# Performance work log

Measured on AMD Instinct MI355X. Metric: run time of the kernel, lower is better.

## Reference

```python
import jax, jax.numpy as jnp
import numpy as np

INV_TEMP = 20.0
THRESHOLD = 0.01
SING_CUTOFF = 3.0
D0 = 128  # order-0 descriptor block
EPS = 1e-6


def setup_inputs() -> dict:
    key = jax.random.key(0)
    ks = jax.random.split(key, 6)
    B, N, M, D = 4, 4096, 4096, 256
    K = (D - D0) // 2
    return {
        "keypoints_A": jax.random.uniform(ks[0], (B, N, 2), jnp.float32) * 2.0 - 1.0,
        "descriptions_A": jax.random.normal(ks[1], (B, N, D), jnp.float32),
        "keypoints_B": jax.random.uniform(ks[2], (B, M, 2), jnp.float32) * 2.0 - 1.0,
        "descriptions_B": jax.random.normal(ks[3], (B, M, D), jnp.float32),
        "W_lstsq": jax.random.normal(ks[4], (D0, K), jnp.float32) * 0.1,
        "b_lstsq": jnp.zeros((K,), jnp.float32),
    }


def _svdvals_2x2(A):
    # singular values of [..,2,2] via eigenvalues of A^T A (closed form)
    M = jnp.einsum('...ki,...kj->...ij', A, A)
    t = M[..., 0, 0] + M[..., 1, 1]
    d = M[..., 0, 0] * M[..., 1, 1] - M[..., 0, 1] * M[..., 1, 0]
    disc = jnp.sqrt(jnp.maximum(0.25 * t * t - d, 0.0))
    lam_hi = 0.5 * t + disc
    lam_lo = jnp.maximum(0.5 * t - disc, 0.0)
    return jnp.sqrt(lam_hi), jnp.sqrt(lam_lo)


def reference(keypoints_A, descriptions_A, keypoints_B, descriptions_B, W_lstsq, b_lstsq):
    B, N, D = descriptions_A.shape
    K = (D - D0) // 2
    # --- dual softmax matcher (normalize=True) ---
    dA = descriptions_A / jnp.linalg.norm(descriptions_A, axis=-1, keepdims=True)
    dB = descriptions_B / jnp.linalg.norm(descriptions_B, axis=-1, keepdims=True)
    sim = INV_TEMP * jnp.einsum('bnd,bmd->bnm', dA, dB)  # [B,N,M]
    P = jax.nn.softmax(sim, axis=-2) * jax.nn.softmax(sim, axis=-1)
    # --- mutual nearest neighbors, fixed-shape (one candidate per A-row) ---
    j = jnp.argmax(P, axis=-1)  # [B,N]
    Pij = jnp.take_along_axis(P, j[..., None], axis=-1)[..., 0]
    colmax_j = jnp.take_along_axis(P.max(axis=-2), j, axis=-1)
    valid = (Pij >= colmax_j) & (Pij > THRESHOLD)  # mutual max + threshold
    # --- gather raw descriptors for matched pairs ---
    descB_m = jnp.take_along_axis(descriptions_B, j[..., None], axis=1)  # [B,N,D]
    desc0_A, desc1_A = descriptions_A[..., :D0], descriptions_A[..., D0:]
    desc0_B, desc1_B = descB_m[..., :D0], descB_m[..., D0:]
    # --- lstsq weights from order-0 features ---
    wA = jax.nn.softplus(desc0_A @ W_lstsq + b_lstsq)
    wB = jax.nn.softplus(desc0_B @ W_lstsq + b_lstsq)
    w = jnp.sqrt(wA * wB)  # [B,N,K]
    # --- weighted 2x2 affine lstsq: A x ~ y ---
    X = desc1_A.reshape(B, N, K, 2)
    Y = desc1_B.reshape(B, N, K, 2)
    G = jnp.einsum('bnk,bnki,bnkj->bnij', w, X, X) + EPS * jnp.eye(2, dtype=X.dtype)
    C = jnp.einsum('bnk,bnki,bnkj->bnij', w, Y, X)
    est = jnp.swapaxes(jnp.linalg.solve(G, jnp.swapaxes(C, -1, -2)), -1, -2)  # [B,N,2,2]
    # --- singular value / determinant filter ---
    s_hi, s_lo = _svdvals_2x2(est)
    good = jnp.isfinite(s_hi + s_lo) & (s_hi < SING_CUTOFF) & (s_lo > 1.0 / SING_CUTOFF)
    det = est[..., 0, 0] * est[..., 1, 1] - est[..., 0, 1] * est[..., 1, 0]
    good = good & (det > 0)  # remove_negative_determinants=True
    valid = valid & good
    matches_A = keypoints_A  # row i of A pairs with column j[b,i]
    matches_B = jnp.take_along_axis(keypoints_B, j[..., None], axis=1)
    return matches_A, matches_B, j, valid
```

## Files before the change

### kernel.cpp

```cpp
#include <hip/hip_runtime.h>
#include <math.h>

#define Bb   4
#define Nn   4096
#define Mm   4096
#define Dd   256
#define D0c  128
#define Kc   64

typedef _Float16 half8 __attribute__((ext_vector_type(8)));
typedef float    f32x4 __attribute__((ext_vector_type(4)));

__device__ __forceinline__ unsigned encf(float f) {
    unsigned u = __float_as_uint(f);
    return (u & 0x80000000u) ? ~u : (u | 0x80000000u);
}
__device__ __forceinline__ float decf(unsigned u) {
    return (u & 0x80000000u) ? __uint_as_float(u ^ 0x80000000u) : __uint_as_float(~u);
}
__device__ __forceinline__ float softplusf(float x) {
    return fmaxf(x, 0.f) + log1pf(expf(-fabsf(x)));
}
__device__ __forceinline__ void gl_lds16(const _Float16* g, _Float16* l) {
    __builtin_amdgcn_global_load_lds((const __attribute__((address_space(1))) void*)g,
                                     (__attribute__((address_space(3))) void*)l, 16, 0, 0);
}

__device__ __forceinline__ void decode_tile(int bid, int swz, int& mt, int& nt, int& zz) {
    if (swz == 2) {
        const int xcd = bid & 7, k = bid >> 3;
        zz = xcd >> 2;
        const int s = xcd & 3;
        mt = (s & 1) * 16 + (k & 15);
        nt = (s >> 1) * 16 + (k >> 4);
    } else if (swz == 1) {
        const int xcd = bid & 7, k = bid >> 3;
        zz = 0;
        const int s = xcd >> 1;
        const int t = (xcd & 1) * 128 + k;
        mt = (s & 1) * 16 + (t & 15);
        nt = (s >> 1) * 16 + (t >> 4);
    } else {
        mt = bid & 31; nt = (bid >> 5) & 31; zz = bid >> 10;
    }
}

__global__ __launch_bounds__(256) void prep_kernel(
    const float* __restrict__ dA, const float* __restrict__ dB,
    _Float16* __restrict__ Ah, _Float16* __restrict__ Al,
    _Float16* __restrict__ Bh, _Float16* __restrict__ Bl,
    unsigned* __restrict__ colMaxU)
{
    const int t = threadIdx.x, wave = t >> 6, lane = t & 63;
    const int row = blockIdx.x * 4 + wave;
    if (blockIdx.y == 0 && lane == 0) colMaxU[row] = 0u;
    const float* src = blockIdx.y ? dB : dA;
    _Float16* dh = blockIdx.y ? Bh : Ah;
    _Float16* dl = blockIdx.y ? Bl : Al;
    const float4 v = *(const float4*)&src[(size_t)row * Dd + lane * 4];
    float ss = v.x * v.x + v.y * v.y + v.z * v.z + v.w * v.w;
#pragma unroll
    for (int m = 32; m; m >>= 1) ss += __shfl_xor(ss, m, 64);
    const float inv = 1.0f / sqrtf(ss);
    float x[4] = {v.x * inv, v.y * inv, v.z * inv, v.w * inv};
    union { _Float16 h[4]; uint2 u; } ph, pl;
#pragma unroll
    for (int i = 0; i < 4; i++) {
        _Float16 h = (_Float16)x[i];
        ph.h[i] = h;
        pl.h[i] = (_Float16)((x[i] - (float)h) * 4096.f);
    }
    const size_t toff = (size_t)(row >> 7) * 32768
                      + (size_t)(lane >> 3) * 4096
                      + (size_t)((lane >> 1) & 3) * 1024
                      + (size_t)(row & 127) * 8 + (lane & 1) * 4;
    *(uint2*)&dh[toff] = ph.u;
    *(uint2*)&dl[toff] = pl.u;
}

template<int PB, int STORE>
__global__ __launch_bounds__(256, 2) void sim_kernel(
    const _Float16* __restrict__ Ah, const _Float16* __restrict__ Al,
    const _Float16* __restrict__ Bh, const _Float16* __restrict__ Bl,
    const float* __restrict__ Lrow_g, const float* __restrict__ Lcol_g,
    float* __restrict__ rowsumP, float* __restrict__ colsumP,
    float* __restrict__ rkey, int* __restrict__ rmArr, float* __restrict__ rcvArr,
    unsigned* __restrict__ cmU, float* __restrict__ simG, int b0, int swz)
{
    __shared__ _Float16 lds[2][4][4][128][8];
    __shared__ float    colp[128];
    __shared__ float    rowp[128];
    __shared__ unsigned colu[128];
    __shared__ float    shL[128], shLc[128];
    __shared__ float    s_bk[128], s_bc[128];
    __shared__ int      s_bm[128];

    const int t = threadIdx.x;
    const int wave = t >> 6, lane = t & 63;
    const int wr = wave >> 1, wc = wave & 1;
    int mt, nt, bbl;
    decode_tile(blockIdx.x, swz, mt, nt, bbl);
    const int bb = b0 + bbl;
    const int n0 = nt * 128, m0 = mt * 128;

    if (PB) {
        if (t < 128) {
            shL[t]  = Lrow_g[bb * Nn + n0 + t];
            shLc[t] = Lcol_g[bb * Mm + m0 + t];
            colu[t] = 0u;
        }
    } else {
        if (t < 128) { colp[t] = 0.f; rowp[t] = 0.f; }
    }

    const _Float16* gb;
    {
        const size_t offA = (size_t)(bb * Nn + n0) * Dd;
        const size_t offB = (size_t)(bb * Mm + m0) * Dd;
        if      (wave == 0) gb = Ah + offA;
        else if (wave == 1) gb = Al + offA;
        else if (wave == 2) gb = Bh + offB;
        else                gb = Bl + offB;
    }

    f32x4 acc1[4][4], acc2[4][4];
#pragma unroll
    for (int ti = 0; ti < 4; ti++)
#pragma unroll
        for (int tj = 0; tj < 4; tj++) { acc1[ti][tj] = (f32x4)0.f; acc2[ti][tj] = (f32x4)0.f; }

    const int quad = lane >> 4, l15 = lane & 15;
    _Float16* lw0 = &lds[0][wave][0][0][0];
    _Float16* lw1 = &lds[1][wave][0][0][0];

#pragma unroll
    for (int q = 0; q < 8; ++q)
        gl_lds16(gb + q * 512 + lane * 8, lw0 + q * 512);

#pragma unroll
    for (int kc8 = 0; kc8 < 8; ++kc8) {
        const int cur = kc8 & 1;
        if (kc8 < 7) {
            _Float16* nw = cur ? lw0 : lw1;
            const _Float16* gsrc = gb + (kc8 + 1) * 4096;
#pragma unroll
            for (int q = 0; q < 8; ++q)
                gl_lds16(gsrc + q * 512 + lane * 8, nw + q * 512);
            asm volatile("s_waitcnt vmcnt(8)" ::: "memory");
        } else {
            asm volatile("s_waitcnt vmcnt(0)" ::: "memory");
        }
        __builtin_amdgcn_s_barrier();
        __builtin_amdgcn_sched_barrier(0);

        half8 afh[4], afl[4];
#pragma unroll
        for (int ti = 0; ti < 4; ++ti) {
            afh[ti] = *(const half8*)&lds[cur][0][quad][wr * 64 + ti * 16 + l15][0];
            afl[ti] = *(const half8*)&lds[cur][1][quad][wr * 64 + ti * 16 + l15][0];
        }
#pragma unroll
        for (int tj = 0; tj < 4; ++tj) {
            half8 bh = *(const half8*)&lds[cur][2][quad][wc * 64 + tj * 16 + l15][0];
            half8 bl = *(const half8*)&lds[cur][3][quad][wc * 64 + tj * 16 + l15][0];
#pragma unroll
            for (int ti = 0; ti < 4; ++ti) {
                acc1[ti][tj] = __builtin_amdgcn_mfma_f32_16x16x32_f16(afh[ti], bh, acc1[ti][tj], 0, 0, 0);
                acc2[ti][tj] = __builtin_amdgcn_mfma_f32_16x16x32_f16(afh[ti], bl, acc2[ti][tj], 0, 0, 0);
                acc2[ti][tj] = __builtin_amdgcn_mfma_f32_16x16x32_f16(afl[ti], bh, acc2[ti][tj], 0, 0, 0);
            }
        }
        asm volatile("s_waitcnt lgkmcnt(0)" ::: "memory");
        __builtin_amdgcn_s_barrier();
    }

    if (!PB) {
        float rp[16] = {0.f}, cp[4] = {0.f};
#pragma unroll
        for (int ti = 0; ti < 4; ++ti)
#pragma unroll
            for (int tj = 0; tj < 4; ++tj)
#pragma unroll
                for (int r = 0; r < 4; ++r) {
                    float dot = fmaf(acc2[ti][tj][r], 2.44140625e-4f, acc1[ti][tj][r]);
                    acc1[ti][tj][r] = dot;
                    float e = __expf(fmaf(20.f, dot, -20.f));
                    rp[ti * 4 + r] += e;
                    cp[tj] += e;
                }
#pragma unroll
        for (int i = 0; i < 16; ++i)
#pragma unroll
            for (int m = 1; m < 16; m <<= 1) rp[i] += __shfl_xor(rp[i], m, 64);
        if (l15 == 0) {
#pragma unroll
            for (int ti = 0; ti < 4; ++ti)
#pragma unroll
                for (int r = 0; r < 4; ++r)
                    atomicAdd(&rowp[wr * 64 + ti * 16 + quad * 4 + r], rp[ti * 4 + r]);
        }
#pragma unroll
        for (int tj = 0; tj < 4; ++tj) {
            cp[tj] += __shfl_xor(cp[tj], 16, 64);
            cp[tj] += __shfl_xor(cp[tj], 32, 64);
        }
        if (quad == 0) {
#pragma unroll
            for (int tj = 0; tj < 4; ++tj) atomicAdd(&colp[wc * 64 + tj * 16 + l15], cp[tj]);
        }
        __syncthreads();
        if (t < 128) {
            rowsumP[(size_t)(bb * 32 + mt) * Nn + n0 + t] = rowp[t];
            colsumP[(size_t)(bb * 32 + nt) * Mm + m0 + t] = colp[t];
        }
        if (STORE) {
            float* base = simG + ((size_t)bbl * Nn + n0) * Mm + m0 + wc * 64;
#pragma unroll
            for (int ti = 0; ti < 4; ++ti)
#pragma unroll
                for (int r = 0; r < 4; ++r) {
                    float* rowp_ = base + (size_t)(wr * 64 + ti * 16 + quad * 4 + r) * Mm;
#pragma unroll
                    for (int tj = 0; tj < 4; ++tj)
                        __builtin_nontemporal_store(acc1[ti][tj][r], rowp_ + tj * 16 + l15);
                }
        }
    } else {
        float Lr[16];
#pragma unroll
        for (int ti = 0; ti < 4; ++ti)
#pragma unroll
            for (int r = 0; r < 4; ++r)
                Lr[ti * 4 + r] = shL[wr * 64 + ti * 16 + quad * 4 + r];

        float bk[16], bc[16];
        int bm[16];
        unsigned cu[4];
#pragma unroll
        for (int i = 0; i < 16; i++) { bk[i] = -INFINITY; bc[i] = -INFINITY; bm[i] = 0x7fffffff; }
#pragma unroll
        for (int j = 0; j < 4; j++) cu[j] = 0u;

#pragma unroll
        for (int ti = 0; ti < 4; ++ti)
#pragma unroll
            for (int tj = 0; tj < 4; ++tj)
#pragma unroll
                for (int r = 0; r < 4; ++r) {
                    float dot = fmaf(acc2[ti][tj][r], 2.44140625e-4f, acc1[ti][tj][r]);
                    float cv = fmaf(40.f, dot, -40.f - Lr[ti * 4 + r]);
                    float kv = cv - shLc[wc * 64 + tj * 16 + l15];
                    const int i = ti * 4 + r;
                    if (kv > bk[i]) { bk[i] = kv; bm[i] = m0 + wc * 64 + tj * 16 + l15; bc[i] = cv; }
                    unsigned e = encf(cv);
                    if (e > cu[tj]) cu[tj] = e;
                }
#pragma unroll
        for (int i = 0; i < 16; ++i) {
#pragma unroll
            for (int m = 1; m < 16; m <<= 1) {
                float okv = __shfl_xor(bk[i], m, 64);
                int   om  = __shfl_xor(bm[i], m, 64);
                float ocv = __shfl_xor(bc[i], m, 64);
                if (okv > bk[i] || (okv == bk[i] && om < bm[i])) { bk[i] = okv; bm[i] = om; bc[i] = ocv; }
            }
        }
        if (l15 == 0 && wc == 0) {
#pragma unroll
            for (int ti = 0; ti < 4; ++ti)
#pragma unroll
                for (int r = 0; r < 4; ++r) {
                    const int row = wr * 64 + ti * 16 + quad * 4 + r, i = ti * 4 + r;
                    s_bk[row] = bk[i]; s_bm[row] = bm[i]; s_bc[row] = bc[i];
                }
        }
        __syncthreads();
        if (l15 == 0 && wc == 1) {
#pragma unroll
            for (int ti = 0; ti < 4; ++ti)
#pragma unroll
                for (int r = 0; r < 4; ++r) {
                    const int row = wr * 64 + ti * 16 + quad * 4 + r, i = ti * 4 + r;
                    float k0 = s_bk[row];
                    if (bk[i] > k0 || (bk[i] == k0 && bm[i] < s_bm[row])) {
                        s_bk[row] = bk[i]; s_bm[row] = bm[i]; s_bc[row] = bc[i];
                    }
                }
        }
#pragma unroll
        for (int tj = 0; tj < 4; ++tj) {
            unsigned o = __shfl_xor(cu[tj], 16, 64); if (o > cu[tj]) cu[tj] = o;
            o = __shfl_xor(cu[tj], 32, 64); if (o > cu[tj]) cu[tj] = o;
        }
        if (quad == 0) {
#pragma unroll
            for (int tj = 0; tj < 4; ++tj) atomicMax(&colu[wc * 64 + tj * 16 + l15], cu[tj]);
        }
        __syncthreads();
        if (t < 128) {
            size_t idx = (size_t)(bb * 32 + mt) * Nn + n0 + t;
            rkey[idx] = s_bk[t]; rmArr[idx] = s_bm[t]; rcvArr[idx] = s_bc[t];
            cmU[(size_t)(bb * 32 + nt) * Mm + m0 + t] = colu[t];
        }
    }
}

__global__ __launch_bounds__(256) void logsum_kernel(
    const float* __restrict__ rowsumP, const float* __restrict__ colsumP,
    float* __restrict__ Lrow, float* __restrict__ Lcol, int b0, int CB)
{
    int t = blockIdx.x * 256 + threadIdx.x;
    int half = CB * 4096;
    int which = t >= half;
    int idx = which ? (t - half) : t;
    int bb = b0 + (idx >> 12), n = idx & 4095;
    const float* P = which ? colsumP : rowsumP;
    float s = 0.f;
    for (int mt = 0; mt < 32; ++mt) s += P[(size_t)(bb * 32 + mt) * 4096 + n];
    (which ? Lcol : Lrow)[bb * 4096 + n] = logf(s);
}

__global__ __launch_bounds__(256) void scan_kernel(
    const float* __restrict__ simG,
    const float* __restrict__ Lrow, const float* __restrict__ Lcol,
    float* __restrict__ kvP, float* __restrict__ cvP, int* __restrict__ jP,
    unsigned* __restrict__ colMaxU, int b0)
{
    __shared__ unsigned colu[1024];
    const int t = threadIdx.x, wave = t >> 6, lane = t & 63;
    const int blk = blockIdx.x;
    const int bbl = blk >> 10;
    const int r10 = blk & 1023;
    const int stripe = r10 >> 2, q = r10 & 3;
    const int bb = b0 + bbl;
    const int col0 = q * 1024;
    const int row0 = stripe * 16 + wave * 4;

    for (int i = t; i < 1024; i += 256) colu[i] = 0u;
    __syncthreads();

    f32x4 Lc4[4], cmax[4];
    const float* LcB = Lcol + bb * Mm + col0;
#pragma unroll
    for (int c = 0; c < 4; ++c) {
        Lc4[c] = *(const f32x4*)&LcB[c * 256 + lane * 4];
        cmax[c] = (f32x4)(-INFINITY);
    }

    const float* rowbase = simG + (size_t)(bbl * Nn + row0) * Mm + col0;
    f32x4 cur[4], nxt[4];
#pragma unroll
    for (int c = 0; c < 4; ++c)
        cur[c] = __builtin_nontemporal_load((const f32x4*)&rowbase[c * 256 + lane * 4]);

    for (int r = 0; r < 4; ++r) {
        if (r < 3) {
            const float* nrow = rowbase + (size_t)(r + 1) * Mm;
#pragma unroll
            for (int c = 0; c < 4; ++c)
                nxt[c] = __builtin_nontemporal_load((const f32x4*)&nrow[c * 256 + lane * 4]);
        }
        const int n = bb * Nn + row0 + r;
        const float Ln = Lrow[n];
        const float cbias = -40.f - Ln;
        float bk = -INFINITY, bc = -INFINITY;
        int bm = 0x7fffffff;
#pragma unroll
        for (int c = 0; c < 4; ++c) {
            float cv0 = fmaf(40.f, cur[c].x, cbias);
            float cv1 = fmaf(40.f, cur[c].y, cbias);
            float cv2 = fmaf(40.f, cur[c].z, cbias);
            float cv3 = fmaf(40.f, cur[c].w, cbias);
            cmax[c].x = fmaxf(cmax[c].x, cv0);
            cmax[c].y = fmaxf(cmax[c].y, cv1);
            cmax[c].z = fmaxf(cmax[c].z, cv2);
            cmax[c].w = fmaxf(cmax[c].w, cv3);
            const int mb = col0 + c * 256 + lane * 4;
            float kv0 = cv0 - Lc4[c].x;
            float kv1 = cv1 - Lc4[c].y;
            float kv2 = cv2 - Lc4[c].z;
            float kv3 = cv3 - Lc4[c].w;
            if (kv0 > bk) { bk = kv0; bm = mb;     bc = cv0; }
            if (kv1 > bk) { bk = kv1; bm = mb + 1; bc = cv1; }
            if (kv2 > bk) { bk = kv2; bm = mb + 2; bc = cv2; }
            if (kv3 > bk) { bk = kv3; bm = mb + 3; bc = cv3; }
        }
#pragma unroll
        for (int sh = 1; sh < 64; sh <<= 1) {
            float okv = __shfl_xor(bk, sh, 64);
            int   om  = __shfl_xor(bm, sh, 64);
            float ocv = __shfl_xor(bc, sh, 64);
            if (okv > bk || (okv == bk && om < bm)) { bk = okv; bm = om; bc = ocv; }
        }
        if (lane == 0) {
            size_t o = ((size_t)bb * Nn + row0 + r) * 4 + q;
            kvP[o] = bk; cvP[o] = bc; jP[o] = bm;
        }
#pragma unroll
        for (int c = 0; c < 4; ++c) cur[c] = nxt[c];
    }
#pragma unroll
    for (int c = 0; c < 4; ++c) {
        const int mb = c * 256 + lane * 4;
        atomicMax(&colu[mb],     encf(cmax[c].x));
        atomicMax(&colu[mb + 1], encf(cmax[c].y));
        atomicMax(&colu[mb + 2], encf(cmax[c].z));
        atomicMax(&colu[mb + 3], encf(cmax[c].w));
    }
    __syncthreads();
    unsigned* cm = colMaxU + (size_t)bb * Mm + col0;
    for (int i = t; i < 1024; i += 256) atomicMax(&cm[i], colu[i]);
}

__global__ __launch_bounds__(256) void validate_kernel(
    const float* __restrict__ kvP, const float* __restrict__ cvP,
    const int* __restrict__ jP, const unsigned* __restrict__ colMaxU,
    float* __restrict__ outJ, int* __restrict__ jIdx, int* __restrict__ v1)
{
    const float LOG_THR = -4.605170185988091f;
    const int p = blockIdx.x * 256 + threadIdx.x;
    const int bb = p >> 12;
    float bk = -INFINITY, bc = -INFINITY;
    int bm = 0x7fffffff;
#pragma unroll
    for (int q = 0; q < 4; ++q) {
        size_t o = (size_t)p * 4 + q;
        float k = kvP[o];
        int   m = jP[o];
        if (k > bk || (k == bk && m < bm)) { bk = k; bm = m; bc = cvP[o]; }
    }
    const float cm = decf(colMaxU[(size_t)bb * Mm + bm]);
    const int ok = (bk > LOG_THR) && (bc >= cm);
    outJ[p] = (float)bm;
    jIdx[p] = bm;
    v1[p] = ok;
}

__global__ __launch_bounds__(256) void finalize_kernel(
    const float* __restrict__ rkey, const int* __restrict__ rmArr,
    const float* __restrict__ rcvArr, const unsigned* __restrict__ cmU,
    float* __restrict__ outJ, int* __restrict__ jIdx, int* __restrict__ v1)
{
    const float LOG_THR = -4.605170185988091f;
    int p = blockIdx.x * 256 + threadIdx.x;
    int bb = p >> 12, n = p & 4095;
    float bk = -INFINITY, bc = -INFINITY;
    int bm = 0;
    for (int mt = 0; mt < 32; ++mt) {
        size_t idx = (size_t)(bb * 32 + mt) * Nn + n;
        float k = rkey[idx];
        if (k > bk) { bk = k; bm = rmArr[idx]; bc = rcvArr[idx]; }
    }
    unsigned u = 0u;
    for (int nt = 0; nt < 32; ++nt) {
        unsigned c = cmU[(size_t)(bb * 32 + nt) * Mm + bm];
        if (c > u) u = c;
    }
    float cm = decf(u);
    int ok = (bk > LOG_THR) && (bc >= cm);
    outJ[p] = (float)bm;
    jIdx[p] = bm;
    v1[p]   = ok;
}

__global__ __launch_bounds__(256) void affine_kernel(
    const float* __restrict__ descA, const float* __restrict__ descB,
    const float* __restrict__ kpA, const float* __restrict__ kpB,
    const float* __restrict__ W, const float* __restrict__ bvec,
    const int* __restrict__ jIdx, const int* __restrict__ v1,
    float* __restrict__ outA, float* __restrict__ outB, float* __restrict__ outV)
{
    __shared__ float Ws[D0c * Kc];
    __shared__ float sbuf[4][4][D0c];
    const int t = threadIdx.x, wave = t >> 6, lane = t & 63;
    for (int i = t; i < D0c * Kc; i += 256) Ws[i] = W[i];
    const float bl = bvec[lane];
    __syncthreads();

    float* s0A = sbuf[wave][0];
    float* s1A = sbuf[wave][1];
    float* s0B = sbuf[wave][2];
    float* s1B = sbuf[wave][3];

    for (int p = 0; p < 8; ++p) {
        const int point = blockIdx.x * 32 + wave * 8 + p;
        const int bb = point >> 12;
        const int j = jIdx[point];
        const float* da = descA + (size_t)point * Dd;
        const float* db = descB + (size_t)(bb * Mm + j) * Dd;
        s0A[lane] = da[lane];       s0A[64 + lane] = da[64 + lane];
        s1A[lane] = da[128 + lane]; s1A[64 + lane] = da[192 + lane];
        s0B[lane] = db[lane];       s0B[64 + lane] = db[64 + lane];
        s1B[lane] = db[128 + lane]; s1B[64 + lane] = db[192 + lane];
        __syncthreads();

        float xa = bl, xb = bl;
#pragma unroll 8
        for (int d = 0; d < 128; ++d) {
            float w_ = Ws[d * 64 + lane];
            xa = fmaf(s0A[d], w_, xa);
            xb = fmaf(s0B[d], w_, xb);
        }
        float wa = softplusf(xa), wb = softplusf(xb);
        float w = sqrtf(wa * wb);
        float x0 = s1A[2 * lane], x1 = s1A[2 * lane + 1];
        float y0 = s1B[2 * lane], y1 = s1B[2 * lane + 1];
        float g00 = w * x0 * x0, g01 = w * x0 * x1, g11 = w * x1 * x1;
        float c00 = w * y0 * x0, c01 = w * y0 * x1;
        float c10 = w * y1 * x0, c11 = w * y1 * x1;
#pragma unroll
        for (int m = 32; m; m >>= 1) {
            g00 += __shfl_xor(g00, m, 64); g01 += __shfl_xor(g01, m, 64); g11 += __shfl_xor(g11, m, 64);
            c00 += __shfl_xor(c00, m, 64); c01 += __shfl_xor(c01, m, 64);
            c10 += __shfl_xor(c10, m, 64); c11 += __shfl_xor(c11, m, 64);
        }
        if (lane == 0) {
            g00 += 1e-6f; g11 += 1e-6f;
            float det = g00 * g11 - g01 * g01;
            float e00 = (c00 * g11 - c01 * g01) / det;
            float e01 = (c01 * g00 - c00 * g01) / det;
            float e10 = (c10 * g11 - c11 * g01) / det;
            float e11 = (c11 * g00 - c10 * g01) / det;
            float m00 = e00 * e00 + e10 * e10;
            float m01 = e00 * e01 + e10 * e11;
            float m11 = e01 * e01 + e11 * e11;
            float tr = m00 + m11;
            float dm = m00 * m11 - m01 * m01;
            float disc = sqrtf(fmaxf(0.25f * tr * tr - dm, 0.f));
            float lhi = 0.5f * tr + disc;
            float llo = fmaxf(0.5f * tr - disc, 0.f);
            float shi = sqrtf(lhi), slo = sqrtf(llo);
            float sdet = e00 * e11 - e01 * e10;
            int good = isfinite(shi + slo) && (shi < 3.0f) && (slo > 0.33333334f) && (sdet > 0.f);
            int valid = v1[point] && good;
            outA[2 * point]     = kpA[2 * point];
            outA[2 * point + 1] = kpA[2 * point + 1];
            const float* kb = kpB + (size_t)(bb * Mm + j) * 2;
            outB[2 * point]     = kb[0];
            outB[2 * point + 1] = kb[1];
            outV[point] = valid ? 1.f : 0.f;
        }
        __syncthreads();
    }
}

extern "C" void kernel_launch(void* const* d_in, const int* in_sizes, int n_in,
                              void* d_out, int out_size, void* d_ws, size_t ws_size,
                              hipStream_t stream) {
    const float* kpA = (const float*)d_in[0];
    const float* dA  = (const float*)d_in[1];
    const float* kpB = (const float*)d_in[2];
    const float* dB  = (const float*)d_in[3];
    const float* W   = (const float*)d_in[4];
    const float* bl  = (const float*)d_in[5];
    float* out = (float*)d_out;

    char* ws = (char*)d_ws;
    _Float16* Ah = (_Float16*)ws;  ws += 8388608;
    _Float16* Al = (_Float16*)ws;  ws += 8388608;
    _Float16* Bh = (_Float16*)ws;  ws += 8388608;
    _Float16* Bl = (_Float16*)ws;  ws += 8388608;
    float*    rowsumP = (float*)ws;    ws += 2097152;
    float*    colsumP = (float*)ws;    ws += 2097152;
    float*    Lrow    = (float*)ws;    ws += 65536;
    float*    Lcol    = (float*)ws;    ws += 65536;
    int*      jIdx    = (int*)ws;      ws += 65536;
    int*      v1      = (int*)ws;      ws += 65536;
    float*    kvP     = (float*)ws;    ws += 262144;
    float*    cvP     = (float*)ws;    ws += 262144;
    int*      jP      = (int*)ws;      ws += 262144;
    unsigned* colMaxU = (unsigned*)ws; ws += 65536;
    char*     big     = ws;

    const size_t base = (size_t)(big - (char*)d_ws);

    float*    rkey  = (float*)big;
    int*      rmArr = (int*)(big + 2097152);
    float*    rcvArr= (float*)(big + 4194304);
    unsigned* cmU   = (unsigned*)(big + 6291456);

    float* outA = out;
    float* outB = out + 32768;
    float* outJ = out + 65536;
    float* outV = out + 81920;

    const size_t per = 67108864ull;
    int CB = 0;
    if      (ws_size >= base + 2 * per) CB = 2;
    else if (ws_size >= base + 1 * per) CB = 1;

    prep_kernel<<<dim3(4096, 2), 256, 0, stream>>>(dA, dB, Ah, Al, Bh, Bl, colMaxU);

    if (CB) {
        float* simG = (float*)big;
        for (int b0 = 0; b0 < Bb; b0 += CB) {
            sim_kernel<0, 1><<<1024 * CB, 256, 0, stream>>>(
                Ah, Al, Bh, Bl, nullptr, nullptr, rowsumP, colsumP,
                nullptr, nullptr, nullptr, nullptr, simG, b0, CB);
            logsum_kernel<<<32 * CB, 256, 0, stream>>>(rowsumP, colsumP, Lrow, Lcol, b0, CB);
            scan_kernel<<<1024 * CB, 256, 0, stream>>>(simG, Lrow, Lcol, kvP, cvP, jP, colMaxU, b0);
        }
        validate_kernel<<<64, 256, 0, stream>>>(kvP, cvP, jP, colMaxU, outJ, jIdx, v1);
    } else {
        sim_kernel<0, 0><<<4096, 256, 0, stream>>>(
            Ah, Al, Bh, Bl, nullptr, nullptr, rowsumP, colsumP,
            nullptr, nullptr, nullptr, nullptr, nullptr, 0, 0);
        logsum_kernel<<<32 * Bb, 256, 0, stream>>>(rowsumP, colsumP, Lrow, Lcol, 0, Bb);
        sim_kernel<1, 0><<<4096, 256, 0, stream>>>(
            Ah, Al, Bh, Bl, Lrow, Lcol, nullptr, nullptr,
            rkey, rmArr, rcvArr, cmU, nullptr, 0, 0);
        finalize_kernel<<<64, 256, 0, stream>>>(rkey, rmArr, rcvArr, cmU, outJ, jIdx, v1);
    }
    affine_kernel<<<512, 256, 0, stream>>>(dA, dB, kpA, kpB, W, bl, jIdx, v1, outA, outB, outV);
}
```

Before: 316.4 us.

## Merge split-precision accumulators, drop LDS double buffering, raise occupancy

After: 304.1 us. 3.9% less time.

```diff
diff --git a/kernel.cpp b/kernel.cpp
--- a/kernel.cpp
+++ b/kernel.cpp
@@ -68,7 +68,7 @@
     for (int i = 0; i < 4; i++) {
         _Float16 h = (_Float16)x[i];
         ph.h[i] = h;
-        pl.h[i] = (_Float16)((x[i] - (float)h) * 4096.f);
+        pl.h[i] = (_Float16)(x[i] - (float)h);
     }
     const size_t toff = (size_t)(row >> 7) * 32768
                       + (size_t)(lane >> 3) * 4096
@@ -79,7 +79,7 @@
 }
 
 template<int PB, int STORE>
-__global__ __launch_bounds__(256, 2) void sim_kernel(
+__global__ __launch_bounds__(256, 3) void sim_kernel(
     const _Float16* __restrict__ Ah, const _Float16* __restrict__ Al,
     const _Float16* __restrict__ Bh, const _Float16* __restrict__ Bl,
     const float* __restrict__ Lrow_g, const float* __restrict__ Lcol_g,
@@ -87,7 +87,7 @@
     float* __restrict__ rkey, int* __restrict__ rmArr, float* __restrict__ rcvArr,
     unsigned* __restrict__ cmU, float* __restrict__ simG, int b0, int swz)
 {
-    __shared__ _Float16 lds[2][4][4][128][8];
+    __shared__ _Float16 lds[4][4][128][8];
     __shared__ float    colp[128];
     __shared__ float    rowp[128];
     __shared__ unsigned colu[128];
@@ -123,55 +123,40 @@
         else                gb = Bl + offB;
     }
 
-    f32x4 acc1[4][4], acc2[4][4];
+    f32x4 acc[4][4];
 #pragma unroll
     for (int ti = 0; ti < 4; ti++)
 #pragma unroll
-        for (int tj = 0; tj < 4; tj++) { acc1[ti][tj] = (f32x4)0.f; acc2[ti][tj] = (f32x4)0.f; }
+        for (int tj = 0; tj < 4; tj++) acc[ti][tj] = (f32x4)0.f;
 
     const int quad = lane >> 4, l15 = lane & 15;
-    _Float16* lw0 = &lds[0][wave][0][0][0];
-    _Float16* lw1 = &lds[1][wave][0][0][0];
-
-#pragma unroll
-    for (int q = 0; q < 8; ++q)
-        gl_lds16(gb + q * 512 + lane * 8, lw0 + q * 512);
-
-#pragma unroll
+    _Float16* ldsw = &lds[wave][0][0][0];
+
     for (int kc8 = 0; kc8 < 8; ++kc8) {
-        const int cur = kc8 & 1;
-        if (kc8 < 7) {
-            _Float16* nw = cur ? lw0 : lw1;
-            const _Float16* gsrc = gb + (kc8 + 1) * 4096;
-#pragma unroll
-            for (int q = 0; q < 8; ++q)
-                gl_lds16(gsrc + q * 512 + lane * 8, nw + q * 512);
-            asm volatile("s_waitcnt vmcnt(8)" ::: "memory");
-        } else {
-            asm volatile("s_waitcnt vmcnt(0)" ::: "memory");
-        }
-        __builtin_amdgcn_s_barrier();
-        __builtin_amdgcn_sched_barrier(0);
+        const _Float16* gsrc = gb + kc8 * 4096;
+#pragma unroll
+        for (int q = 0; q < 8; ++q)
+            gl_lds16(gsrc + q * 512 + lane * 8, ldsw + q * 512);
+        __syncthreads();
 
         half8 afh[4], afl[4];
 #pragma unroll
         for (int ti = 0; ti < 4; ++ti) {
-            afh[ti] = *(const half8*)&lds[cur][0][quad][wr * 64 + ti * 16 + l15][0];
-            afl[ti] = *(const half8*)&lds[cur][1][quad][wr * 64 + ti * 16 + l15][0];
+            afh[ti] = *(const half8*)&lds[0][quad][wr * 64 + ti * 16 + l15][0];
+            afl[ti] = *(const half8*)&lds[1][quad][wr * 64 + ti * 16 + l15][0];
         }
 #pragma unroll
         for (int tj = 0; tj < 4; ++tj) {
-            half8 bh = *(const half8*)&lds[cur][2][quad][wc * 64 + tj * 16 + l15][0];
-            half8 bl = *(const half8*)&lds[cur][3][quad][wc * 64 + tj * 16 + l15][0];
+            half8 bh = *(const half8*)&lds[2][quad][wc * 64 + tj * 16 + l15][0];
+            half8 bl = *(const half8*)&lds[3][quad][wc * 64 + tj * 16 + l15][0];
 #pragma unroll
             for (int ti = 0; ti < 4; ++ti) {
-                acc1[ti][tj] = __builtin_amdgcn_mfma_f32_16x16x32_f16(afh[ti], bh, acc1[ti][tj], 0, 0, 0);
-                acc2[ti][tj] = __builtin_amdgcn_mfma_f32_16x16x32_f16(afh[ti], bl, acc2[ti][tj], 0, 0, 0);
-                acc2[ti][tj] = __builtin_amdgcn_mfma_f32_16x16x32_f16(afl[ti], bh, acc2[ti][tj], 0, 0, 0);
+                acc[ti][tj] = __builtin_amdgcn_mfma_f32_16x16x32_f16(afh[ti], bh, acc[ti][tj], 0, 0, 0);
+                acc[ti][tj] = __builtin_amdgcn_mfma_f32_16x16x32_f16(afh[ti], bl, acc[ti][tj], 0, 0, 0);
+                acc[ti][tj] = __builtin_amdgcn_mfma_f32_16x16x32_f16(afl[ti], bh, acc[ti][tj], 0, 0, 0);
             }
         }
-        asm volatile("s_waitcnt lgkmcnt(0)" ::: "memory");
-        __builtin_amdgcn_s_barrier();
+        __syncthreads();
     }
 
     if (!PB) {
@@ -182,9 +167,7 @@
             for (int tj = 0; tj < 4; ++tj)
 #pragma unroll
                 for (int r = 0; r < 4; ++r) {
-                    float dot = fmaf(acc2[ti][tj][r], 2.44140625e-4f, acc1[ti][tj][r]);
-                    acc1[ti][tj][r] = dot;
-                    float e = __expf(fmaf(20.f, dot, -20.f));
+                    float e = __expf(fmaf(20.f, acc[ti][tj][r], -20.f));
                     rp[ti * 4 + r] += e;
                     cp[tj] += e;
                 }
@@ -222,7 +205,7 @@
                     float* rowp_ = base + (size_t)(wr * 64 + ti * 16 + quad * 4 + r) * Mm;
 #pragma unroll
                     for (int tj = 0; tj < 4; ++tj)
-                        __builtin_nontemporal_store(acc1[ti][tj][r], rowp_ + tj * 16 + l15);
+                        __builtin_nontemporal_store(acc[ti][tj][r], rowp_ + tj * 16 + l15);
                 }
         }
     } else {
@@ -247,8 +230,7 @@
             for (int tj = 0; tj < 4; ++tj)
 #pragma unroll
                 for (int r = 0; r < 4; ++r) {
-                    float dot = fmaf(acc2[ti][tj][r], 2.44140625e-4f, acc1[ti][tj][r]);
-                    float cv = fmaf(40.f, dot, -40.f - Lr[ti * 4 + r]);
+                    float cv = fmaf(40.f, acc[ti][tj][r], -40.f - Lr[ti * 4 + r]);
                     float kv = cv - shLc[wc * 64 + tj * 16 + l15];
                     const int i = ti * 4 + r;
                     if (kv > bk[i]) { bk[i] = kv; bm[i] = m0 + wc * 64 + tj * 16 + l15; bc[i] = cv; }
```
